# Performance work log

Measured on AMD Instinct MI355X. Metric: run time of the kernel, lower is better.

Reference implementation:

```python
import jax, jax.numpy as jnp
import numpy as np

N, E, D_IN, D_HID, D_OUT = 50000, 800000, 128, 128, 128


def setup_inputs() -> dict:
    key = jax.random.key(0)
    ks = jax.random.split(key, 10)
    x = jax.random.normal(ks[0], (N, D_IN), dtype=jnp.float32)
    edge_index = jax.random.randint(ks[1], (2, E), 0, N, dtype=jnp.int64)
    def xavier(k, fan_in, fan_out):
        lim = jnp.sqrt(6.0 / (fan_in + fan_out)).astype(jnp.float32)
        return jax.random.uniform(k, (fan_in, fan_out), jnp.float32, -lim, lim)
    return {
        "x": x,
        "edge_index": edge_index,
        "W1l": xavier(ks[2], D_IN, D_HID), "b1l": jnp.zeros((D_HID,), jnp.float32),
        "W1r": xavier(ks[3], D_IN, D_HID),
        "W2l": xavier(ks[4], D_HID, D_OUT), "b2l": jnp.zeros((D_OUT,), jnp.float32),
        "W2r": xavier(ks[5], D_HID, D_OUT),
        "Wfc": xavier(ks[6], D_OUT, 2), "bfc": jnp.zeros((2,), jnp.float32),
    }


def _mean_aggregate(x, src, dst, num_nodes):
    # gather neighbor (source) features, scatter-mean to destination nodes
    msgs = x[src]                                        # [E, D]
    summed = jax.ops.segment_sum(msgs, dst, num_segments=num_nodes)
    ones = jnp.ones((src.shape[0],), x.dtype)
    counts = jax.ops.segment_sum(ones, dst, num_segments=num_nodes)
    return summed / jnp.maximum(counts, 1.0)[:, None]


def _l2_normalize(x, eps=1e-12):
    # matches torch F.normalize(p=2, dim=-1): divide by clamp(norm, min=eps)
    norm = jnp.sqrt(jnp.sum(x * x, axis=-1, keepdims=True))
    return x / jnp.maximum(norm, eps)


def _sage_conv(x, src, dst, Wl, bl, Wr):
    agg = _mean_aggregate(x, src, dst, x.shape[0])
    out = agg @ Wl + bl + x @ Wr
    return _l2_normalize(out)


def reference(x, edge_index, W1l, b1l, W1r, W2l, b2l, W2r, Wfc, bfc):
    src, dst = edge_index[0], edge_index[1]  # PyG: row=source(j), col=target(i)
    h = _sage_conv(x, src, dst, W1l, b1l, W1r)
    h = jax.nn.relu(h)
    h = _sage_conv(h, src, dst, W2l, b2l, W2r)
    logits = h @ Wfc + bfc
    return jax.nn.softmax(logits, axis=-1)
```

## Files before the change

### kernel.cpp

```cpp
#include <hip/hip_runtime.h>

#define D 128
#define CBITS 8

typedef __attribute__((ext_vector_type(8))) short short8;
typedef __attribute__((ext_vector_type(4))) float f32x4;

__device__ __forceinline__ unsigned short f2b(float f) {
    unsigned u = __builtin_bit_cast(unsigned, f);
    u += 0x7fffu + ((u >> 16) & 1u);
    return (unsigned short)(u >> 16);
}
__device__ __forceinline__ float b2f(unsigned short b) {
    unsigned u = ((unsigned)b) << 16;
    return __builtin_bit_cast(float, u);
}


__global__ __launch_bounds__(256) void prep_kernel(
    const float* __restrict__ x, unsigned short* __restrict__ acat, int nCast, int n8,
    const float* __restrict__ W1l, const float* __restrict__ W1r,
    const float* __restrict__ W2l, const float* __restrict__ W2r,
    unsigned short* __restrict__ WT1, unsigned short* __restrict__ WT2,
    int4* __restrict__ zeroPtr, int* __restrict__ offsets, int nnodes, int E) {
    const int b = blockIdx.x;
    if (b < nCast) {
        int g = b * 256 + threadIdx.x;
        if (g < n8) {
            int row = g >> 4, chunk = g & 15;
            const float4 v0 = *reinterpret_cast<const float4*>(x + (size_t)g * 8);
            const float4 v1 = *reinterpret_cast<const float4*>(x + (size_t)g * 8 + 4);
            short8 r;
            r[0] = (short)f2b(v0.x); r[1] = (short)f2b(v0.y); r[2] = (short)f2b(v0.z); r[3] = (short)f2b(v0.w);
            r[4] = (short)f2b(v1.x); r[5] = (short)f2b(v1.y); r[6] = (short)f2b(v1.z); r[7] = (short)f2b(v1.w);
            *reinterpret_cast<short8*>(acat + (size_t)row * 256 + 128 + chunk * 8) = r;
        }
    } else if (b < nCast + 256) {
        int bb = b - nCast;
        int layer = bb >> 7;
        int j = bb & 127;
        int k = threadIdx.x;
        const float* Wl = layer ? W2l : W1l;
        const float* Wr = layer ? W2r : W1r;
        unsigned short* WT = layer ? WT2 : WT1;
        float v = (k < 128) ? Wl[k * D + j] : Wr[(k - 128) * D + j];
        WT[(size_t)j * 256 + k] = f2b(v);
    } else {
        if (threadIdx.x < 128) zeroPtr[threadIdx.x] = make_int4(0, 0, 0, 0);
        if (threadIdx.x == 0) offsets[nnodes] = E;
    }
}


__global__ __launch_bounds__(256) void bucket_count_kernel(
    const int* __restrict__ dst, int* __restrict__ bucketCnt, int E) {
    __shared__ int hist[256];
    const int t = threadIdx.x;
    hist[t] = 0;
    __syncthreads();
    const int base = blockIdx.x * 4096;
#pragma unroll
    for (int i = 0; i < 16; ++i) {
        int e = base + i * 256 + t;
        if (e < E) atomicAdd(&hist[dst[e] >> CBITS], 1);
    }
    __syncthreads();
    if (hist[t]) atomicAdd(&bucketCnt[t], hist[t]);
}

__global__ __launch_bounds__(256) void bin_coarse_kernel(
    const int* __restrict__ src, const int* __restrict__ dst,
    const int* __restrict__ bucketCnt, int* __restrict__ cursorA,
    int* __restrict__ staging, int E) {

    __shared__ int hist[256];
    __shared__ int lcur[256];
    const int t = threadIdx.x;

    int cnt = bucketCnt[t];
    lcur[t] = cnt;
    __syncthreads();
    for (int d = 1; d < 256; d <<= 1) {
        int u = (t >= d) ? lcur[t - d] : 0;
        __syncthreads();
        lcur[t] += u;
        __syncthreads();
    }
    const int myBase = lcur[t] - cnt;
    __syncthreads();

    hist[t] = 0;
    __syncthreads();

    const int base = blockIdx.x * 4096;
    int sreg[16], dreg[16];
#pragma unroll
    for (int i = 0; i < 16; ++i) {
        int e = base + i * 256 + t;
        int s = 0, d = -1;
        if (e < E) {
            s = src[e]; d = dst[e];
            atomicAdd(&hist[d >> CBITS], 1);
        }
        sreg[i] = s; dreg[i] = d;
    }
    __syncthreads();
    {
        int h = hist[t];
        lcur[t] = myBase + (h ? atomicAdd(&cursorA[t], h) : 0);
    }
    __syncthreads();
#pragma unroll
    for (int i = 0; i < 16; ++i) {
        if (dreg[i] >= 0) {
            int p = atomicAdd(&lcur[dreg[i] >> CBITS], 1);
            staging[p] = sreg[i] | ((dreg[i] & 255) << 16);
        }
    }
}

__global__ __launch_bounds__(256) void bucket_build_kernel(
    const int* __restrict__ staging, const int* __restrict__ bucketCnt,
    int* __restrict__ offsets, int* __restrict__ csr, int nnodes) {

    __shared__ int A1[256];
    __shared__ int A2[256];
    const int t = threadIdx.x;
    const int b = blockIdx.x;

    int cnt = bucketCnt[t];
    A1[t] = cnt;
    __syncthreads();
    for (int d = 1; d < 256; d <<= 1) {
        int u = (t >= d) ? A1[t - d] : 0;
        __syncthreads();
        A1[t] += u;
        __syncthreads();
    }
    const int end  = A1[b];
    const int base = end - bucketCnt[b];
    __syncthreads();

    A1[t] = 0;
    __syncthreads();
    for (int i = base + t; i < end; i += 256)
        atomicAdd(&A1[(staging[i] >> 16) & 255], 1);
    __syncthreads();
    A2[t] = A1[t];
    __syncthreads();
    for (int d = 1; d < 256; d <<= 1) {
        int u = (t >= d) ? A2[t - d] : 0;
        __syncthreads();
        A2[t] += u;
        __syncthreads();
    }
    const int excl = A2[t] - A1[t];
    const int node = (b << CBITS) + t;
    if (node < nnodes) offsets[node] = base + excl;
    __syncthreads();
    A1[t] = base + excl;
    __syncthreads();
    for (int i = base + t; i < end; i += 256) {
        int p = staging[i];
        int c = atomicAdd(&A1[(p >> 16) & 255], 1);
        csr[c] = p & 0xFFFF;
    }
}


__global__ __launch_bounds__(256) void aggregate_kernel(
    const unsigned short* __restrict__ xin,
    const int* __restrict__ offsets, const int* __restrict__ csr,
    unsigned short* __restrict__ out,
    int nnodes) {
    int node = blockIdx.x * 16 + (threadIdx.x >> 4);
    int l16 = threadIdx.x & 15;
    if (node >= nnodes) return;
    int lo = offsets[node], hi = offsets[node + 1];
    float acc[8] = {0.f, 0.f, 0.f, 0.f, 0.f, 0.f, 0.f, 0.f};
    int k = lo;
    for (; k + 8 <= hi; k += 8) {
        int s[8];
        short8 v[8];
#pragma unroll
        for (int u = 0; u < 8; ++u) s[u] = csr[k + u];
#pragma unroll
        for (int u = 0; u < 8; ++u)
            v[u] = *reinterpret_cast<const short8*>(xin + (size_t)s[u] * 256 + l16 * 8);
#pragma unroll
        for (int u = 0; u < 8; ++u)
#pragma unroll
            for (int i = 0; i < 8; ++i) acc[i] += b2f((unsigned short)v[u][i]);
    }
    for (; k < hi; ++k) {
        int s = csr[k];
        const short8 v = *reinterpret_cast<const short8*>(xin + (size_t)s * 256 + l16 * 8);
#pragma unroll
        for (int i = 0; i < 8; ++i) acc[i] += b2f((unsigned short)v[i]);
    }
    float inv = 1.0f / fmaxf((float)(hi - lo), 1.0f);
    short8 r;
#pragma unroll
    for (int i = 0; i < 8; ++i) r[i] = (short)f2b(acc[i] * inv);
    *reinterpret_cast<short8*>(out + (size_t)node * 256 + l16 * 8) = r;
}


template <bool RELU, bool HEAD>
__global__ __launch_bounds__(256) void sage_mfma_kernel(
    const unsigned short* __restrict__ Acat, const unsigned short* __restrict__ WT,
    const float* __restrict__ bias, unsigned short* __restrict__ hout, int out_stride,
    const float* __restrict__ Wfc, const float* __restrict__ bfc,
    float* __restrict__ outf, int nnodes) {

    __shared__ unsigned short Blds[128 * 256];
    const int tid = threadIdx.x;

    {
        const short8* wsrc = reinterpret_cast<const short8*>(WT);
#pragma unroll
        for (int it = 0; it < 16; ++it) {
            int u = it * 256 + tid;
            int row = u >> 5, c = u & 31;
            int cs = c ^ (row & 7);
            *reinterpret_cast<short8*>(
                reinterpret_cast<char*>(Blds) + row * 512 + cs * 16) = wsrc[u];
        }
    }
    __syncthreads();

    const int w = tid >> 6, l = tid & 63;
    const int r16 = l & 15, g = l >> 4;
    const int rowbase = blockIdx.x * 128 + w * 32;

    f32x4 acc[2][8];
#pragma unroll
    for (int j = 0; j < 8; ++j) {
        float bj = bias[j * 16 + r16];
        acc[0][j] = (f32x4){bj, bj, bj, bj};
        acc[1][j] = (f32x4){bj, bj, bj, bj};
    }

    const unsigned short* ap0 = Acat + (size_t)(rowbase + r16) * 256 + g * 8;
    const unsigned short* ap1 = ap0 + 16 * 256;

#pragma unroll
    for (int ks = 0; ks < 8; ++ks) {
        const short8 a0 = *reinterpret_cast<const short8*>(ap0 + ks * 32);
        const short8 a1 = *reinterpret_cast<const short8*>(ap1 + ks * 32);
        const int cs = ((ks * 4 + g) ^ (r16 & 7)) * 16;
#pragma unroll
        for (int j = 0; j < 8; ++j) {
            const short8 b = *reinterpret_cast<const short8*>(
                reinterpret_cast<const char*>(Blds) + (j * 16 + r16) * 512 + cs);
            acc[0][j] = __builtin_amdgcn_mfma_f32_16x16x32_bf16(a0, b, acc[0][j], 0, 0, 0);
            acc[1][j] = __builtin_amdgcn_mfma_f32_16x16x32_bf16(a1, b, acc[1][j], 0, 0, 0);
        }
    }

#pragma unroll
    for (int rb = 0; rb < 2; ++rb) {
        float ss[4] = {0.f, 0.f, 0.f, 0.f};
#pragma unroll
        for (int j = 0; j < 8; ++j)
#pragma unroll
            for (int i = 0; i < 4; ++i) ss[i] += acc[rb][j][i] * acc[rb][j][i];
#pragma unroll
        for (int m = 1; m < 16; m <<= 1)
#pragma unroll
            for (int i = 0; i < 4; ++i) ss[i] += __shfl_xor(ss[i], m, 64);

        if (!HEAD) {
#pragma unroll
            for (int i = 0; i < 4; ++i) {
                int row = rowbase + rb * 16 + g * 4 + i;
                if (row >= nnodes) continue;
                float sc = 1.0f / fmaxf(sqrtf(ss[i]), 1e-12f);
#pragma unroll
                for (int j = 0; j < 8; ++j) {
                    float v = acc[rb][j][i] * sc;
                    if (RELU) v = fmaxf(v, 0.f);
                    hout[(size_t)row * out_stride + j * 16 + r16] = f2b(v);
                }
            }
        } else {
            float w0[8], w1[8];
#pragma unroll
            for (int j = 0; j < 8; ++j) {
                const float2 wv = *reinterpret_cast<const float2*>(Wfc + (j * 16 + r16) * 2);
                w0[j] = wv.x; w1[j] = wv.y;
            }
            const float b0 = bfc[0], b1 = bfc[1];
#pragma unroll
            for (int i = 0; i < 4; ++i) {
                float sc = 1.0f / fmaxf(sqrtf(ss[i]), 1e-12f);
                float l0 = 0.f, l1 = 0.f;
#pragma unroll
                for (int j = 0; j < 8; ++j) {
                    float v = acc[rb][j][i] * sc;
                    l0 = fmaf(v, w0[j], l0);
                    l1 = fmaf(v, w1[j], l1);
                }
#pragma unroll
                for (int m = 1; m < 16; m <<= 1) {
                    l0 += __shfl_xor(l0, m, 64);
                    l1 += __shfl_xor(l1, m, 64);
                }
                int row = rowbase + rb * 16 + g * 4 + i;
                if (r16 == 0 && row < nnodes) {
                    float d0 = l0 + b0, d1 = l1 + b1;
                    float mx = fmaxf(d0, d1);
                    float e0 = expf(d0 - mx), e1 = expf(d1 - mx);
                    float inv = 1.0f / (e0 + e1);
                    outf[(size_t)row * 2]     = e0 * inv;
                    outf[(size_t)row * 2 + 1] = e1 * inv;
                }
            }
        }
    }
}


extern "C" void kernel_launch(void* const* d_in, const int* in_sizes, int n_in,
                              void* d_out, int out_size, void* d_ws, size_t ws_size,
                              hipStream_t stream) {
    const float* x   = (const float*)d_in[0];
    const int*   ei  = (const int*)d_in[1];
    const float* W1l = (const float*)d_in[2];
    const float* b1l = (const float*)d_in[3];
    const float* W1r = (const float*)d_in[4];
    const float* W2l = (const float*)d_in[5];
    const float* b2l = (const float*)d_in[6];
    const float* W2r = (const float*)d_in[7];
    const float* Wfc = (const float*)d_in[8];
    const float* bfc = (const float*)d_in[9];

    const int N = in_sizes[0] / D;
    const int E = in_sizes[1] / 2;
    const int* src = ei;
    const int* dst = ei + E;
    const int NBC = (N + (1 << CBITS) - 1) >> CBITS;

    unsigned short* Acat1 = (unsigned short*)d_ws;
    unsigned short* Acat2 = Acat1 + (size_t)N * 256;
    int* staging          = (int*)Acat2;
    unsigned short* WT1   = Acat2 + (size_t)N * 256;
    unsigned short* WT2   = WT1 + 128 * 256;
    int* bucketCnt  = (int*)(WT2 + 128 * 256);
    int* cursorA    = bucketCnt + 256;
    int* offsets    = cursorA + 256;
    int* csr        = offsets + N + 1;

    const int nCast = (N * 16 + 255) / 256;

    prep_kernel<<<nCast + 256 + 1, 256, 0, stream>>>(
        x, Acat1, nCast, N * 16, W1l, W1r, W2l, W2r, WT1, WT2,
        (int4*)bucketCnt, offsets, N, E);

    bucket_count_kernel<<<(E + 4095) / 4096, 256, 0, stream>>>(dst, bucketCnt, E);
    bin_coarse_kernel<<<(E + 4095) / 4096, 256, 0, stream>>>(src, dst, bucketCnt, cursorA, staging, E);
    bucket_build_kernel<<<NBC, 256, 0, stream>>>(staging, bucketCnt, offsets, csr, N);

    aggregate_kernel<<<(N + 15) / 16, 256, 0, stream>>>(Acat1 + 128, offsets, csr, Acat1, N);
    sage_mfma_kernel<true, false><<<(N + 127) / 128, 256, 0, stream>>>(
        Acat1, WT1, b1l, Acat2 + 128, 256, nullptr, nullptr, nullptr, N);

    aggregate_kernel<<<(N + 15) / 16, 256, 0, stream>>>(Acat2 + 128, offsets, csr, Acat2, N);
    sage_mfma_kernel<false, true><<<(N + 127) / 128, 256, 0, stream>>>(
        Acat2, WT2, b2l, nullptr, 0, Wfc, bfc, (float*)d_out, N);
}
```

Before: 133.2 us.

## Fold bucket histogram into prep kernel and store CSR indices as 16-bit

Moves the per-block destination histogram into extra blocks of the prep kernel, writing a per-block histogram matrix instead of using global atomics. Consumers now sum that matrix themselves, which removes one kernel launch and the zeroing dependency. CSR source indices are narrowed to unsigned short, halving index traffic in both aggregation passes. The narrowing relies on N fitting in 16 bits, and each consumer block now re-reads about 196 histogram rows.

New measurement: 160.2 us. 20.2% more time.

```diff
diff --git a/kernel.cpp b/kernel.cpp
--- a/kernel.cpp
+++ b/kernel.cpp
@@ -22,10 +22,12 @@
     const float* __restrict__ W1l, const float* __restrict__ W1r,
     const float* __restrict__ W2l, const float* __restrict__ W2r,
     unsigned short* __restrict__ WT1, unsigned short* __restrict__ WT2,
-    int4* __restrict__ zeroPtr, int* __restrict__ offsets, int nnodes, int E) {
+    int4* __restrict__ zeroPtr, int* __restrict__ offsets, int nnodes, int E,
+    const int* __restrict__ dst, int* __restrict__ histMat) {
     const int b = blockIdx.x;
+    const int t = threadIdx.x;
     if (b < nCast) {
-        int g = b * 256 + threadIdx.x;
+        int g = b * 256 + t;
         if (g < n8) {
             int row = g >> 4, chunk = g & 15;
             const float4 v0 = *reinterpret_cast<const float4*>(x + (size_t)g * 8);
@@ -39,45 +41,42 @@
         int bb = b - nCast;
         int layer = bb >> 7;
         int j = bb & 127;
-        int k = threadIdx.x;
         const float* Wl = layer ? W2l : W1l;
         const float* Wr = layer ? W2r : W1r;
         unsigned short* WT = layer ? WT2 : WT1;
-        float v = (k < 128) ? Wl[k * D + j] : Wr[(k - 128) * D + j];
-        WT[(size_t)j * 256 + k] = f2b(v);
+        float v = (t < 128) ? Wl[t * D + j] : Wr[(t - 128) * D + j];
+        WT[(size_t)j * 256 + t] = f2b(v);
+    } else if (b == nCast + 256) {
+        if (t < 64) zeroPtr[t] = make_int4(0, 0, 0, 0);
+        if (t == 0) offsets[nnodes] = E;
     } else {
-        if (threadIdx.x < 128) zeroPtr[threadIdx.x] = make_int4(0, 0, 0, 0);
-        if (threadIdx.x == 0) offsets[nnodes] = E;
-    }
-}
-
-
-__global__ __launch_bounds__(256) void bucket_count_kernel(
-    const int* __restrict__ dst, int* __restrict__ bucketCnt, int E) {
-    __shared__ int hist[256];
-    const int t = threadIdx.x;
-    hist[t] = 0;
-    __syncthreads();
-    const int base = blockIdx.x * 4096;
-#pragma unroll
-    for (int i = 0; i < 16; ++i) {
-        int e = base + i * 256 + t;
-        if (e < E) atomicAdd(&hist[dst[e] >> CBITS], 1);
-    }
-    __syncthreads();
-    if (hist[t]) atomicAdd(&bucketCnt[t], hist[t]);
-}
+        __shared__ int hist[256];
+        hist[t] = 0;
+        __syncthreads();
+        const int hb = b - nCast - 257;
+        const int base = hb * 4096;
+#pragma unroll
+        for (int i = 0; i < 16; ++i) {
+            int e = base + i * 256 + t;
+            if (e < E) atomicAdd(&hist[dst[e] >> CBITS], 1);
+        }
+        __syncthreads();
+        histMat[hb * 256 + t] = hist[t];
+    }
+}
+
 
 __global__ __launch_bounds__(256) void bin_coarse_kernel(
     const int* __restrict__ src, const int* __restrict__ dst,
-    const int* __restrict__ bucketCnt, int* __restrict__ cursorA,
+    const int* __restrict__ histMat, int nHist, int* __restrict__ cursorA,
     int* __restrict__ staging, int E) {
 
     __shared__ int hist[256];
     __shared__ int lcur[256];
     const int t = threadIdx.x;
 
-    int cnt = bucketCnt[t];
+    int cnt = 0;
+    for (int r = 0; r < nHist; ++r) cnt += histMat[r * 256 + t];
     lcur[t] = cnt;
     __syncthreads();
     for (int d = 1; d < 256; d <<= 1) {
@@ -120,15 +119,16 @@
 }
 
 __global__ __launch_bounds__(256) void bucket_build_kernel(
-    const int* __restrict__ staging, const int* __restrict__ bucketCnt,
-    int* __restrict__ offsets, int* __restrict__ csr, int nnodes) {
+    const int* __restrict__ staging, const int* __restrict__ histMat, int nHist,
+    int* __restrict__ offsets, unsigned short* __restrict__ csr, int nnodes) {
 
     __shared__ int A1[256];
     __shared__ int A2[256];
     const int t = threadIdx.x;
     const int b = blockIdx.x;
 
-    int cnt = bucketCnt[t];
+    int cnt = 0;
+    for (int r = 0; r < nHist; ++r) cnt += histMat[r * 256 + t];
     A1[t] = cnt;
     __syncthreads();
     for (int d = 1; d < 256; d <<= 1) {
@@ -138,7 +138,7 @@
         __syncthreads();
     }
     const int end  = A1[b];
-    const int base = end - bucketCnt[b];
+    const int base = end - ((b == 0) ? A1[0] : (A1[b] - A1[b - 1]));
     __syncthreads();
 
     A1[t] = 0;
@@ -163,14 +163,14 @@
     for (int i = base + t; i < end; i += 256) {
         int p = staging[i];
         int c = atomicAdd(&A1[(p >> 16) & 255], 1);
-        csr[c] = p & 0xFFFF;
+        csr[c] = (unsigned short)(p & 0xFFFF);
     }
 }
 
 
 __global__ __launch_bounds__(256) void aggregate_kernel(
     const unsigned short* __restrict__ xin,
-    const int* __restrict__ offsets, const int* __restrict__ csr,
+    const int* __restrict__ offsets, const unsigned short* __restrict__ csr,
     unsigned short* __restrict__ out,
     int nnodes) {
     int node = blockIdx.x * 16 + (threadIdx.x >> 4);
@@ -340,26 +340,26 @@
     const int* src = ei;
     const int* dst = ei + E;
     const int NBC = (N + (1 << CBITS) - 1) >> CBITS;
+    const int nHist = (E + 4095) / 4096;
 
     unsigned short* Acat1 = (unsigned short*)d_ws;
     unsigned short* Acat2 = Acat1 + (size_t)N * 256;
     int* staging          = (int*)Acat2;
     unsigned short* WT1   = Acat2 + (size_t)N * 256;
     unsigned short* WT2   = WT1 + 128 * 256;
-    int* bucketCnt  = (int*)(WT2 + 128 * 256);
-    int* cursorA    = bucketCnt + 256;
-    int* offsets    = cursorA + 256;
-    int* csr        = offsets + N + 1;
+    int* cursorA    = (int*)(WT2 + 128 * 256);
+    int* histMat    = cursorA + 256;
+    int* offsets    = histMat + (size_t)nHist * 256;
+    unsigned short* csr = (unsigned short*)(offsets + N + 1);
 
     const int nCast = (N * 16 + 255) / 256;
 
-    prep_kernel<<<nCast + 256 + 1, 256, 0, stream>>>(
+    prep_kernel<<<nCast + 256 + 1 + nHist, 256, 0, stream>>>(
         x, Acat1, nCast, N * 16, W1l, W1r, W2l, W2r, WT1, WT2,
-        (int4*)bucketCnt, offsets, N, E);
-
-    bucket_count_kernel<<<(E + 4095) / 4096, 256, 0, stream>>>(dst, bucketCnt, E);
-    bin_coarse_kernel<<<(E + 4095) / 4096, 256, 0, stream>>>(src, dst, bucketCnt, cursorA, staging, E);
-    bucket_build_kernel<<<NBC, 256, 0, stream>>>(staging, bucketCnt, offsets, csr, N);
+        (int4*)cursorA, offsets, N, E, dst, histMat);
+
+    bin_coarse_kernel<<<nHist, 256, 0, stream>>>(src, dst, histMat, nHist, cursorA, staging, E);
+    bucket_build_kernel<<<NBC, 256, 0, stream>>>(staging, histMat, nHist, offsets, csr, N);
 
     aggregate_kernel<<<(N + 15) / 16, 256, 0, stream>>>(Acat1 + 128, offsets, csr, Acat1, N);
     sage_mfma_kernel<true, false><<<(N + 127) / 128, 256, 0, stream>>>(
```
